# Kernel tuning notes

Hardware: AMD Instinct MI355X
Metric: run time of the kernel (lower is better)

The kernel has to match this reference:

```python
import jax, jax.numpy as jnp
import numpy as np

N = 50000      # nodes
E = 800000     # edges (before self loops)
D_IN = 128
D_H = 128
HEADS = 4
C = D_H // HEADS
D_OUT = 64
G = 50         # graphs in batch
EPS = 1e-5


def setup_inputs() -> dict:
    key = jax.random.key(0)
    ks = jax.random.split(key, 40)
    def rn(k, shape, scale=0.05):
        return jax.random.normal(k, shape, jnp.float32) * scale
    inp = {}
    inp['x'] = jax.random.normal(ks[0], (N, D_IN), jnp.float32)
    inp['edge_index'] = jax.random.randint(ks[1], (2, E), 0, N, dtype=jnp.int32)
    inp['batch'] = jnp.sort(jax.random.randint(ks[2], (N,), 0, G, dtype=jnp.int32))
    # GATConv 1 (in=D_IN, heads=4, out-per-head=C, concat)
    inp['gat1_W'] = rn(ks[3], (D_IN, D_H))
    inp['gat1_as'] = rn(ks[4], (HEADS, C))
    inp['gat1_ad'] = rn(ks[5], (HEADS, C))
    inp['gat1_b'] = rn(ks[6], (D_H,))
    # GATConv 2 (in=D_H)
    inp['gat2_W'] = rn(ks[7], (D_H, D_H))
    inp['gat2_as'] = rn(ks[8], (HEADS, C))
    inp['gat2_ad'] = rn(ks[9], (HEADS, C))
    inp['gat2_b'] = rn(ks[10], (D_H,))
    # SAGEConv 3/4/5: lin_l (aggregated neighbors, has bias), lin_r (root, no bias)
    for i, kk in zip((3, 4, 5), (11, 14, 17)):
        inp[f'sage{i}_Wl'] = rn(ks[kk], (D_H, D_H))
        inp[f'sage{i}_bl'] = rn(ks[kk + 1], (D_H,))
        inp[f'sage{i}_Wr'] = rn(ks[kk + 2], (D_H, D_H))
    # BatchNorms (training-mode batch statistics)
    for i in range(1, 6):
        inp[f'bn{i}_g'] = jnp.ones((D_H,), jnp.float32)
        inp[f'bn{i}_b'] = jnp.zeros((D_H,), jnp.float32)
    # residual projections + final fc
    inp['res1_W'] = rn(ks[20], (D_IN, D_H)); inp['res1_b'] = rn(ks[21], (D_H,))
    inp['res2_W'] = rn(ks[22], (D_H, D_H)); inp['res2_b'] = rn(ks[23], (D_H,))
    inp['fc_W'] = rn(ks[24], (D_H, D_OUT)); inp['fc_b'] = rn(ks[25], (D_OUT,))
    return inp


def _segsum(v, idx, n):
    return jax.ops.segment_sum(v, idx, num_segments=n)


def _gat(x, W, a_src, a_dst, b, src, dst):
    # PyG GATConv with self loops already appended to (src, dst).
    h = (x @ W).reshape(N, HEADS, C)
    es = jnp.einsum('nhc,hc->nh', h, a_src)           # [N,H]
    ed = jnp.einsum('nhc,hc->nh', h, a_dst)
    e = jax.nn.leaky_relu(es[src] + ed[dst], 0.2)     # [Etot,H]
    m = jax.ops.segment_max(e, dst, num_segments=N)
    m = jnp.where(jnp.isfinite(m), m, 0.0)
    w = jnp.exp(e - m[dst])
    z = _segsum(w, dst, N)
    alpha = w / jnp.maximum(z[dst], 1e-16)            # edge softmax over dst
    out = _segsum(h[src] * alpha[:, :, None], dst, N)  # [N,H,C]
    return out.reshape(N, D_H) + b


def _sage(x, Wl, bl, Wr, src, dst):
    # PyG SAGEConv(aggr='mean'): lin_l(mean_neighbors) + lin_r(x)
    deg = _segsum(jnp.ones((src.shape[0],), x.dtype), dst, N)
    mean = _segsum(x[src], dst, N) / jnp.maximum(deg, 1.0)[:, None]
    return mean @ Wl + bl + x @ Wr


def _bn(x, g, b):
    mu = x.mean(0)
    var = x.var(0)
    return g * (x - mu) * jax.lax.rsqrt(var + EPS) + b


def reference(x, edge_index, batch,
              gat1_W, gat1_as, gat1_ad, gat1_b,
              gat2_W, gat2_as, gat2_ad, gat2_b,
              sage3_Wl, sage3_bl, sage3_Wr,
              sage4_Wl, sage4_bl, sage4_Wr,
              sage5_Wl, sage5_bl, sage5_Wr,
              bn1_g, bn1_b, bn2_g, bn2_b, bn3_g, bn3_b, bn4_g, bn4_b, bn5_g, bn5_b,
              res1_W, res1_b, res2_W, res2_b, fc_W, fc_b):
    src, dst = edge_index[0], edge_index[1]
    loops = jnp.arange(N, dtype=edge_index.dtype)
    gsrc = jnp.concatenate([src, loops])   # GATConv adds self loops by default
    gdst = jnp.concatenate([dst, loops])
    lrelu = lambda v: jax.nn.leaky_relu(v, 0.2)

    res1 = x @ res1_W + res1_b
    h = _gat(x, gat1_W, gat1_as, gat1_ad, gat1_b, gsrc, gdst)
    h = lrelu(_bn(h, bn1_g, bn1_b) + res1)            # dropout = identity (eval)

    res2 = h @ res2_W + res2_b
    h = _gat(h, gat2_W, gat2_as, gat2_ad, gat2_b, gsrc, gdst)
    h = lrelu(_bn(h, bn2_g, bn2_b) + res2)

    h = lrelu(_bn(_sage(h, sage3_Wl, sage3_bl, sage3_Wr, src, dst), bn3_g, bn3_b))
    h = lrelu(_bn(_sage(h, sage4_Wl, sage4_bl, sage4_Wr, src, dst), bn4_g, bn4_b))
    h = lrelu(_bn(_sage(h, sage5_Wl, sage5_bl, sage5_Wr, src, dst), bn5_g, bn5_b))

    # global_mean_pool over graphs
    cnt = jax.ops.segment_sum(jnp.ones((N,), h.dtype), batch, num_segments=G)
    pooled = jax.ops.segment_sum(h, batch, num_segments=G) / jnp.maximum(cnt, 1.0)[:, None]
    return pooled @ fc_W + fc_b
```

## Files before the change

kernel.cpp:

```cpp
#include <hip/hip_runtime.h>
#include <math.h>
#include <stdint.h>

#define N_NODES 50000
#define N_EDGES 800000
#define D 128
#define GR 50
#define EPSV 1e-5f
#define GATGRID 2048

typedef __attribute__((ext_vector_type(8))) short bf16x8;
typedef __attribute__((ext_vector_type(4))) float f32x4;

__device__ __forceinline__ float lrelu(float v){ return v > 0.f ? v : 0.2f*v; }

__device__ __forceinline__ unsigned int f2bf(float f){
  union { float f; uint32_t i; } v; v.f = f;
  uint32_t r = v.i + 0x7fffu + ((v.i >> 16) & 1u);
  return r >> 16;
}
__device__ __forceinline__ float2 bf2f2(uint32_t u){
  union { uint32_t i; float f; } a, b;
  a.i = u << 16;
  b.i = u & 0xffff0000u;
  return make_float2(a.f, b.f);
}

__global__ void k_countrank(const int* __restrict__ dst, int* __restrict__ deg,
                            int* __restrict__ rank){
  int e = blockIdx.x*256 + threadIdx.x;
  if (e < N_EDGES) rank[e] = atomicAdd(&deg[dst[e]], 1);
}
__global__ void k_scan1(const int* __restrict__ deg, int* __restrict__ bsum){
  __shared__ int s[256];
  int i = blockIdx.x*256 + threadIdx.x;
  int v = (i < N_NODES) ? deg[i] : 0;
  s[threadIdx.x] = v; __syncthreads();
  for (int off = 128; off > 0; off >>= 1){
    if (threadIdx.x < off) s[threadIdx.x] += s[threadIdx.x + off];
    __syncthreads();
  }
  if (threadIdx.x == 0) bsum[blockIdx.x] = s[0];
}
__global__ void k_scan2b(int* __restrict__ bsum, int nb, int* __restrict__ rowStart){
  __shared__ int s[256];
  int t = threadIdx.x;
  int v = (t < nb) ? bsum[t] : 0;
  s[t] = v; __syncthreads();
  for (int off = 1; off < 256; off <<= 1){
    int xv = (t >= off) ? s[t - off] : 0;
    __syncthreads();
    s[t] += xv;
    __syncthreads();
  }
  if (t < nb) bsum[t] = s[t] - v;
  if (t == 255) rowStart[N_NODES] = s[255];
}
__global__ void k_scan3(const int* __restrict__ deg, const int* __restrict__ bsum,
                        int* __restrict__ rowStart){
  __shared__ int s[256];
  int i = blockIdx.x*256 + threadIdx.x;
  int v = (i < N_NODES) ? deg[i] : 0;
  s[threadIdx.x] = v; __syncthreads();
  for (int off = 1; off < 256; off <<= 1){
    int xv = (threadIdx.x >= off) ? s[threadIdx.x - off] : 0;
    __syncthreads();
    s[threadIdx.x] += xv;
    __syncthreads();
  }
  if (i < N_NODES) rowStart[i] = bsum[blockIdx.x] + s[threadIdx.x] - v;
}
__global__ void k_scatter(const int* __restrict__ src, const int* __restrict__ dst,
                          const int* __restrict__ rank, const int* __restrict__ rowStart,
                          int* __restrict__ srcList){
  int e = blockIdx.x*256 + threadIdx.x;
  if (e < N_EDGES)
    srcList[rowStart[dst[e]] + rank[e]] = src[e];
}

__global__ void k_cast_x(const float* __restrict__ x, unsigned short* __restrict__ x16){
  int idx = blockIdx.x*256 + threadIdx.x;
  if (idx >= N_NODES*32) return;
  float4 v = *(const float4*)(x + (size_t)idx*4);
  uint2 pk;
  pk.x = f2bf(v.x) | (f2bf(v.y) << 16);
  pk.y = f2bf(v.z) | (f2bf(v.w) << 16);
  *(uint2*)(x16 + (size_t)idx*4) = pk;
}

struct WPack { const float* w[10]; };
__global__ void k_castw(WPack p, unsigned short* __restrict__ wt){
  int mat = blockIdx.x >> 6;
  int local = (blockIdx.x & 63)*256 + threadIdx.x;
  int c = local >> 7, k = local & 127;
  wt[(size_t)mat*16384 + c*128 + k] = (unsigned short)f2bf(p.w[mat][k*128 + c]);
}

__device__ __forceinline__ void stage_w(const unsigned short* __restrict__ wt,
                                        unsigned short* __restrict__ lds, int t){
  #pragma unroll
  for (int i = 0; i < 8; ++i){
    int ch = i*256 + t;
    int col = ch >> 4, kc = ch & 15;
    *(uint4*)(&lds[col*136 + kc*8]) = *(const uint4*)(wt + ((size_t)col << 7) + (kc << 3));
  }
}

__device__ __forceinline__ void load_a(const unsigned short* __restrict__ xrow,
                                       int quad, bf16x8 a[4]){
  #pragma unroll
  for (int ks = 0; ks < 4; ++ks)
    a[ks] = *(const bf16x8*)(xrow + ks*32 + quad*8);
}

__device__ __forceinline__ void mfma_regs(const bf16x8 a[4],
                                          const unsigned short* __restrict__ lds,
                                          int lane, f32x4 acc[8]){
  int quad = lane >> 4, m = lane & 15;
  #pragma unroll
  for (int ks = 0; ks < 4; ++ks){
    #pragma unroll
    for (int nt = 0; nt < 8; ++nt){
      bf16x8 b = *(const bf16x8*)(&lds[(nt*16 + m)*136 + ks*32 + quad*8]);
      acc[nt] = __builtin_amdgcn_mfma_f32_16x16x32_bf16(a[ks], b, acc[nt], 0, 0, 0);
    }
  }
}

__device__ __forceinline__ void epi_store16(f32x4 acc[8], const float* bias,
    unsigned short* __restrict__ ldsw, unsigned short* __restrict__ Y16,
    int rbase, int lane, int n){
  int quad = lane >> 4, m = lane & 15;
  #pragma unroll
  for (int nt = 0; nt < 8; ++nt){
    int col = nt*16 + m;
    float bv = bias ? bias[col] : 0.f;
    #pragma unroll
    for (int reg = 0; reg < 4; ++reg)
      ldsw[(quad*4 + reg)*132 + col] = (unsigned short)f2bf(acc[nt][reg] + bv);
  }
  int r = lane >> 2, seg = lane & 3;
  int grow = rbase + r;
  if (grow < n){
    unsigned short* gp = Y16 + (size_t)grow*128 + seg*32;
    #pragma unroll
    for (int j = 0; j < 4; ++j)
      *(uint4*)(gp + j*8) = *(const uint4*)(&ldsw[r*132 + seg*32 + j*8]);
  }
}

__global__ __launch_bounds__(256) void k_mgemm_dual(const unsigned short* __restrict__ X16,
    const unsigned short* __restrict__ wtres, const unsigned short* __restrict__ wtgat,
    const float* __restrict__ bres, const float* __restrict__ as_,
    const float* __restrict__ ad_, unsigned short* __restrict__ R16,
    unsigned short* __restrict__ H16, float* __restrict__ es, float* __restrict__ ed,
    int n){
  __shared__ __align__(16) unsigned short Wlds[128*136];
  int t = threadIdx.x, lane = t & 63, w = t >> 6;
  int quad = lane >> 4, m = lane & 15;
  int rbase = blockIdx.x*64 + w*16;
  int rowA = rbase + m; if (rowA >= n) rowA = n - 1;
  bf16x8 a[4];
  load_a(X16 + (size_t)rowA*128, quad, a);
  stage_w(wtres, Wlds, t);
  f32x4 accR[8], accG[8];
  #pragma unroll
  for (int nt = 0; nt < 8; ++nt){
    accR[nt][0]=0.f; accR[nt][1]=0.f; accR[nt][2]=0.f; accR[nt][3]=0.f;
    accG[nt][0]=0.f; accG[nt][1]=0.f; accG[nt][2]=0.f; accG[nt][3]=0.f;
  }
  __syncthreads();
  mfma_regs(a, Wlds, lane, accR);
  __syncthreads();
  stage_w(wtgat, Wlds, t);
  __syncthreads();
  mfma_regs(a, Wlds, lane, accG);

  float asv[8], adv[8];
  #pragma unroll
  for (int nt = 0; nt < 8; ++nt){ asv[nt] = as_[nt*16 + m]; adv[nt] = ad_[nt*16 + m]; }
  #pragma unroll
  for (int reg = 0; reg < 4; ++reg){
    int row = rbase + quad*4 + reg;
    float pe[4], pd[4];
    #pragma unroll
    for (int h = 0; h < 4; ++h){
      pe[h] = accG[2*h][reg]*asv[2*h] + accG[2*h+1][reg]*asv[2*h+1];
      pd[h] = accG[2*h][reg]*adv[2*h] + accG[2*h+1][reg]*adv[2*h+1];
    }
    #pragma unroll
    for (int h = 0; h < 4; ++h){
      pe[h] += __shfl_xor(pe[h], 1); pe[h] += __shfl_xor(pe[h], 2);
      pe[h] += __shfl_xor(pe[h], 4); pe[h] += __shfl_xor(pe[h], 8);
      pd[h] += __shfl_xor(pd[h], 1); pd[h] += __shfl_xor(pd[h], 2);
      pd[h] += __shfl_xor(pd[h], 4); pd[h] += __shfl_xor(pd[h], 8);
    }
    if (m == 0 && row < n){
      #pragma unroll
      for (int h = 0; h < 4; ++h){ es[row*4 + h] = pe[h]; ed[row*4 + h] = pd[h]; }
    }
  }
  __syncthreads();
  epi_store16(accR, bres,    Wlds + w*2112, R16, rbase, lane, n);
  epi_store16(accG, nullptr, Wlds + w*2112, H16, rbase, lane, n);
}

__global__ __launch_bounds__(256) void k_mgemm2(const unsigned short* __restrict__ Xa,
    const unsigned short* __restrict__ wta, const unsigned short* __restrict__ Xb,
    const unsigned short* __restrict__ wtb, const float* __restrict__ bias,
    unsigned short* __restrict__ Y16, int n, float* __restrict__ bnpart){
  __shared__ __align__(16) unsigned short Wlds[128*136];
  __shared__ float wredS[4][128], wredQ[4][128];
  int t = threadIdx.x, lane = t & 63, w = t >> 6;
  int quad = lane >> 4, m = lane & 15;
  int rbase = blockIdx.x*64 + w*16;
  int rowA = rbase + m; if (rowA >= n) rowA = n - 1;
  bf16x8 aa[4], ab[4];
  load_a(Xa + (size_t)rowA*128, quad, aa);
  load_a(Xb + (size_t)rowA*128, quad, ab);
  stage_w(wta, Wlds, t);
  f32x4 acc[8];
  #pragma unroll
  for (int nt = 0; nt < 8; ++nt){ acc[nt][0]=0.f; acc[nt][1]=0.f; acc[nt][2]=0.f; acc[nt][3]=0.f; }
  __syncthreads();
  mfma_regs(aa, Wlds, lane, acc);
  __syncthreads();
  stage_w(wtb, Wlds, t);
  __syncthreads();
  mfma_regs(ab, Wlds, lane, acc);

  float colS[8], colQ[8];
  #pragma unroll
  for (int nt = 0; nt < 8; ++nt){
    float bv = bias[nt*16 + m];
    float s = 0.f, q = 0.f;
    #pragma unroll
    for (int reg = 0; reg < 4; ++reg){
      float o = acc[nt][reg] + bv;
      acc[nt][reg] = o;
      if (rbase + quad*4 + reg < n){ s += o; q += o*o; }
    }
    s += __shfl_xor(s, 16); s += __shfl_xor(s, 32);
    q += __shfl_xor(q, 16); q += __shfl_xor(q, 32);
    colS[nt] = s; colQ[nt] = q;
  }
  if (quad == 0){
    #pragma unroll
    for (int nt = 0; nt < 8; ++nt){
      wredS[w][nt*16 + m] = colS[nt];
      wredQ[w][nt*16 + m] = colQ[nt];
    }
  }
  __syncthreads();
  if (t < 128){
    float S = wredS[0][t] + wredS[1][t] + wredS[2][t] + wredS[3][t];
    float Q = wredQ[0][t] + wredQ[1][t] + wredQ[2][t] + wredQ[3][t];
    bnpart[(size_t)blockIdx.x*256 + t]       = S;
    bnpart[(size_t)blockIdx.x*256 + 128 + t] = Q;
  }
  epi_store16(acc, nullptr, Wlds + w*2112, Y16, rbase, lane, n);
}

__global__ void k_bnred(const float* __restrict__ part, int nblk,
                        float* __restrict__ sums){
  int g = blockIdx.x, t = threadIdx.x;
  int chunk = (nblk + 63) / 64;
  int b0 = g*chunk, b1 = min(nblk, b0 + chunk);
  float s = 0.f;
  for (int b = b0; b < b1; ++b) s += part[(size_t)b*256 + t];
  if (b0 < b1) atomicAdd(&sums[t], s);
}

__global__ __launch_bounds__(256) void k_gat(const uint4* __restrict__ h16,
    const float* __restrict__ es, const float* __restrict__ edv,
    const int* __restrict__ rowStart, const int* __restrict__ srcList,
    const float* __restrict__ bias, uint4* __restrict__ out16,
    float* __restrict__ bnpart){
  __shared__ float wredS[4][128], wredQ[4][128];
  int t = threadIdx.x;
  int lane = t & 63, wv = t >> 6;
  int sub = lane >> 4;
  int m   = lane & 15;
  int hd  = m >> 2;
  float4 bv0 = *(const float4*)(bias + m*8);
  float4 bv1 = *(const float4*)(bias + m*8 + 4);
  float colS[8], colQ[8];
  #pragma unroll
  for (int j = 0; j < 8; ++j){ colS[j] = 0.f; colQ[j] = 0.f; }

  for (int i = blockIdx.x*4 + wv; i < N_NODES; i += GATGRID*4){
    float edi = edv[i*4 + hd];
    float acc[8];
    #pragma unroll
    for (int j = 0; j < 8; ++j) acc[j] = 0.f;
    float z = 0.f;
    if (sub == 0){
      float ws = __expf(lrelu(es[i*4 + hd] + edi));
      uint4 u = h16[i*16 + m];
      float2 v0=bf2f2(u.x), v1=bf2f2(u.y), v2=bf2f2(u.z), v3=bf2f2(u.w);
      acc[0]=v0.x*ws; acc[1]=v0.y*ws; acc[2]=v1.x*ws; acc[3]=v1.y*ws;
      acc[4]=v2.x*ws; acc[5]=v2.y*ws; acc[6]=v3.x*ws; acc[7]=v3.y*ws;
      z = ws;
    }
    int k0 = rowStart[i], ke = rowStart[i + 1];
    for (int k = k0; k < ke; k += 8){
      int e0 = k + sub, e1 = k + 4 + sub;
      int c0 = e0 < ke ? e0 : ke - 1;
      int c1 = e1 < ke ? e1 : ke - 1;
      int s0 = srcList[c0];
      int s1 = srcList[c1];
      uint4 u0 = h16[s0*16 + m];
      uint4 u1 = h16[s1*16 + m];
      float w0 = (e0 < ke) ? __expf(lrelu(es[s0*4 + hd] + edi)) : 0.f;
      float w1 = (e1 < ke) ? __expf(lrelu(es[s1*4 + hd] + edi)) : 0.f;
      z += w0 + w1;
      float2 a0=bf2f2(u0.x), a1=bf2f2(u0.y), a2=bf2f2(u0.z), a3=bf2f2(u0.w);
      float2 b0=bf2f2(u1.x), b1=bf2f2(u1.y), b2=bf2f2(u1.z), b3=bf2f2(u1.w);
      acc[0] += a0.x*w0 + b0.x*w1;  acc[1] += a0.y*w0 + b0.y*w1;
      acc[2] += a1.x*w0 + b1.x*w1;  acc[3] += a1.y*w0 + b1.y*w1;
      acc[4] += a2.x*w0 + b2.x*w1;  acc[5] += a2.y*w0 + b2.y*w1;
      acc[6] += a3.x*w0 + b3.x*w1;  acc[7] += a3.y*w0 + b3.y*w1;
    }
    #pragma unroll
    for (int j = 0; j < 8; ++j){
      acc[j] += __shfl_xor(acc[j], 16);
      acc[j] += __shfl_xor(acc[j], 32);
    }
    z += __shfl_xor(z, 16);
    z += __shfl_xor(z, 32);
    if (sub == 0){
      float inv = 1.f / z;
      float o[8];
      o[0]=acc[0]*inv+bv0.x; o[1]=acc[1]*inv+bv0.y; o[2]=acc[2]*inv+bv0.z; o[3]=acc[3]*inv+bv0.w;
      o[4]=acc[4]*inv+bv1.x; o[5]=acc[5]*inv+bv1.y; o[6]=acc[6]*inv+bv1.z; o[7]=acc[7]*inv+bv1.w;
      #pragma unroll
      for (int j = 0; j < 8; ++j){ colS[j] += o[j]; colQ[j] += o[j]*o[j]; }
      uint4 pk;
      pk.x = f2bf(o[0]) | (f2bf(o[1]) << 16);
      pk.y = f2bf(o[2]) | (f2bf(o[3]) << 16);
      pk.z = f2bf(o[4]) | (f2bf(o[5]) << 16);
      pk.w = f2bf(o[6]) | (f2bf(o[7]) << 16);
      out16[i*16 + m] = pk;
    }
  }
  if (sub == 0){
    #pragma unroll
    for (int j = 0; j < 8; ++j){
      wredS[wv][m*8 + j] = colS[j];
      wredQ[wv][m*8 + j] = colQ[j];
    }
  }
  __syncthreads();
  if (t < 128){
    float S = wredS[0][t] + wredS[1][t] + wredS[2][t] + wredS[3][t];
    float Q = wredQ[0][t] + wredQ[1][t] + wredQ[2][t] + wredQ[3][t];
    bnpart[(size_t)blockIdx.x*256 + t]       = S;
    bnpart[(size_t)blockIdx.x*256 + 128 + t] = Q;
  }
}

__global__ __launch_bounds__(256) void k_sage_mean(const uint4* __restrict__ h16,
    const int* __restrict__ rowStart, const int* __restrict__ srcList,
    uint4* __restrict__ out16){
  int i = blockIdx.x*4 + (threadIdx.x >> 6);
  if (i >= N_NODES) return;
  int lane = threadIdx.x & 63;
  int sub = lane >> 4;
  int m   = lane & 15;
  float acc[8];
  #pragma unroll
  for (int j = 0; j < 8; ++j) acc[j] = 0.f;
  int k0 = rowStart[i], ke = rowStart[i + 1];
  for (int k = k0; k < ke; k += 8){
    int e0 = k + sub, e1 = k + 4 + sub;
    int c0 = e0 < ke ? e0 : ke - 1;
    int c1 = e1 < ke ? e1 : ke - 1;
    int s0 = srcList[c0];
    int s1 = srcList[c1];
    uint4 u0 = h16[s0*16 + m];
    uint4 u1 = h16[s1*16 + m];
    float w0 = (e0 < ke) ? 1.f : 0.f;
    float w1 = (e1 < ke) ? 1.f : 0.f;
    float2 a0=bf2f2(u0.x), a1=bf2f2(u0.y), a2=bf2f2(u0.z), a3=bf2f2(u0.w);
    float2 b0=bf2f2(u1.x), b1=bf2f2(u1.y), b2=bf2f2(u1.z), b3=bf2f2(u1.w);
    acc[0] += a0.x*w0 + b0.x*w1;  acc[1] += a0.y*w0 + b0.y*w1;
    acc[2] += a1.x*w0 + b1.x*w1;  acc[3] += a1.y*w0 + b1.y*w1;
    acc[4] += a2.x*w0 + b2.x*w1;  acc[5] += a2.y*w0 + b2.y*w1;
    acc[6] += a3.x*w0 + b3.x*w1;  acc[7] += a3.y*w0 + b3.y*w1;
  }
  #pragma unroll
  for (int j = 0; j < 8; ++j){
    acc[j] += __shfl_xor(acc[j], 16);
    acc[j] += __shfl_xor(acc[j], 32);
  }
  if (sub == 0){
    int dg = ke - k0;
    float inv = 1.f / (float)(dg > 0 ? dg : 1);
    uint4 pk;
    pk.x = f2bf(acc[0]*inv) | (f2bf(acc[1]*inv) << 16);
    pk.y = f2bf(acc[2]*inv) | (f2bf(acc[3]*inv) << 16);
    pk.z = f2bf(acc[4]*inv) | (f2bf(acc[5]*inv) << 16);
    pk.w = f2bf(acc[6]*inv) | (f2bf(acc[7]*inv) << 16);
    out16[i*16 + m] = pk;
  }
}

__global__ void k_bnapply(const unsigned int* __restrict__ x16,
    const float* __restrict__ sums, const float* __restrict__ g,
    const float* __restrict__ b, const unsigned int* __restrict__ res16,
    unsigned int* __restrict__ y16){
  int f = blockIdx.x*256 + threadIdx.x;
  if (f >= N_NODES*32) return;
  int c = (f & 31) * 4;
  uint2 u = *(const uint2*)(x16 + (size_t)f*2);
  float2 vA = bf2f2(u.x), vB = bf2f2(u.y);
  float vv[4] = {vA.x, vA.y, vB.x, vB.y};
  float rr[4] = {0.f, 0.f, 0.f, 0.f};
  if (res16){
    uint2 ur = *(const uint2*)(res16 + (size_t)f*2);
    float2 rA = bf2f2(ur.x), rB = bf2f2(ur.y);
    rr[0]=rA.x; rr[1]=rA.y; rr[2]=rB.x; rr[3]=rB.y;
  }
  float o[4];
  const float invn = 1.f / (float)N_NODES;
  #pragma unroll
  for (int j = 0; j < 4; ++j){
    int cc = c + j;
    float mu  = sums[cc] * invn;
    float var = sums[128 + cc] * invn - mu*mu;
    float rs  = rsqrtf(var + EPSV);
    o[j] = lrelu((vv[j] - mu)*rs*g[cc] + b[cc] + rr[j]);
  }
  uint2 pk;
  pk.x = f2bf(o[0]) | (f2bf(o[1]) << 16);
  pk.y = f2bf(o[2]) | (f2bf(o[3]) << 16);
  *(uint2*)(y16 + (size_t)f*2) = pk;
}

__global__ __launch_bounds__(256) void k_pool(const unsigned int* __restrict__ h16,
    const int* __restrict__ batch, float* __restrict__ pooled,
    float* __restrict__ cnt){
  int colu = threadIdx.x & 63;
  int ro   = threadIdx.x >> 6;
  int base = blockIdx.x * 128;
  int g_cur = -1; float a0 = 0.f, a1 = 0.f, cacc = 0.f;
  for (int ii = 0; ii < 32; ++ii){
    int r = base + ro + ii*4;
    if (r >= N_NODES) break;
    int g = batch[r];
    if (g != g_cur){
      if (g_cur >= 0){
        atomicAdd(&pooled[g_cur*D + 2*colu],     a0);
        atomicAdd(&pooled[g_cur*D + 2*colu + 1], a1);
        if (colu == 0) atomicAdd(&cnt[g_cur], cacc);
      }
      a0 = 0.f; a1 = 0.f; cacc = 0.f; g_cur = g;
    }
    float2 v = bf2f2(h16[(size_t)r*64 + colu]);
    a0 += v.x; a1 += v.y; cacc += 1.f;
  }
  if (g_cur >= 0){
    atomicAdd(&pooled[g_cur*D + 2*colu],     a0);
    atomicAdd(&pooled[g_cur*D + 2*colu + 1], a1);
    if (colu == 0) atomicAdd(&cnt[g_cur], cacc);
  }
}

__global__ void k_fc(const float* __restrict__ pooled, const float* __restrict__ cnt,
    const float* __restrict__ W, const float* __restrict__ b, float* __restrict__ out){
  int idx = blockIdx.x*256 + threadIdx.x;
  if (idx >= GR*64) return;
  int g = idx >> 6, o = idx & 63;
  const float* p = pooled + g*D;
  float s = 0.f;
  for (int c2 = 0; c2 < D; ++c2) s += p[c2] * W[c2*64 + o];
  float inv = 1.f / fmaxf(cnt[g], 1.f);
  out[idx] = s*inv + b[o];
}

extern "C" void kernel_launch(void* const* d_in, const int* in_sizes, int n_in,
                              void* d_out, int out_size, void* d_ws, size_t ws_size,
                              hipStream_t stream){
  (void)in_sizes; (void)n_in; (void)out_size; (void)ws_size;
  const float* x       = (const float*)d_in[0];
  const int*   ei      = (const int*)  d_in[1];
  const int*   batch   = (const int*)  d_in[2];
  const float* gat1_W  = (const float*)d_in[3];
  const float* gat1_as = (const float*)d_in[4];
  const float* gat1_ad = (const float*)d_in[5];
  const float* gat1_b  = (const float*)d_in[6];
  const float* gat2_W  = (const float*)d_in[7];
  const float* gat2_as = (const float*)d_in[8];
  const float* gat2_ad = (const float*)d_in[9];
  const float* gat2_b  = (const float*)d_in[10];
  const float* s3_Wl   = (const float*)d_in[11];
  const float* s3_bl   = (const float*)d_in[12];
  const float* s3_Wr   = (const float*)d_in[13];
  const float* s4_Wl   = (const float*)d_in[14];
  const float* s4_bl   = (const float*)d_in[15];
  const float* s4_Wr   = (const float*)d_in[16];
  const float* s5_Wl   = (const float*)d_in[17];
  const float* s5_bl   = (const float*)d_in[18];
  const float* s5_Wr   = (const float*)d_in[19];
  const float* bn1_g = (const float*)d_in[20]; const float* bn1_b = (const float*)d_in[21];
  const float* bn2_g = (const float*)d_in[22]; const float* bn2_b = (const float*)d_in[23];
  const float* bn3_g = (const float*)d_in[24]; const float* bn3_b = (const float*)d_in[25];
  const float* bn4_g = (const float*)d_in[26]; const float* bn4_b = (const float*)d_in[27];
  const float* bn5_g = (const float*)d_in[28]; const float* bn5_b = (const float*)d_in[29];
  const float* res1_W = (const float*)d_in[30]; const float* res1_b = (const float*)d_in[31];
  const float* res2_W = (const float*)d_in[32]; const float* res2_b = (const float*)d_in[33];
  const float* fc_W   = (const float*)d_in[34]; const float* fc_b   = (const float*)d_in[35];
  float* out = (float*)d_out;

  char* ws = (char*)d_ws;
  size_t off = 0;
  auto alloc = [&](size_t bytes) -> void* {
    void* p = ws + off; off += (bytes + 255) & ~(size_t)255; return p;
  };
  const int mgrid = (N_NODES + 63) / 64;
  int*   rowStart = (int*)  alloc((N_NODES + 1) * 4);
  int*   deg      = (int*)  alloc((size_t)N_NODES * 4);
  int*   rank     = (int*)  alloc((size_t)N_EDGES * 4);
  int*   srcList  = (int*)  alloc((size_t)N_EDGES * 4);
  int*   bsum     = (int*)  alloc(256 * 4);
  float* bnsums   = (float*)alloc(5 * 256 * 4);
  float* pooled   = (float*)alloc(GR * D * 4);
  float* cnt      = (float*)alloc(64 * 4);
  float* es       = (float*)alloc((size_t)N_NODES * 4 * 4);
  float* edv      = (float*)alloc((size_t)N_NODES * 4 * 4);
  float* bnpart   = (float*)alloc((size_t)GATGRID * 256 * 4);
  unsigned short* Wt16 = (unsigned short*)alloc(10 * 16384 * 2);
  unsigned short* HX   = (unsigned short*)alloc((size_t)N_NODES * D * 2);
  unsigned short* H16a = (unsigned short*)alloc((size_t)N_NODES * D * 2);
  unsigned short* HO   = (unsigned short*)alloc((size_t)N_NODES * D * 2);
  unsigned short* HR   = (unsigned short*)alloc((size_t)N_NODES * D * 2);

  const int* srcE = ei;
  const int* dstE = ei + N_EDGES;
  const int nb = (N_NODES + 255) / 256;
  const int egrid = (N_EDGES + 255) / 256;
  const int agrid = (N_NODES + 3) / 4;
  const int bgrid = (N_NODES*32 + 255) / 256;
  const int pgrid = (N_NODES + 127) / 128;

  hipMemsetAsync(deg, 0, (size_t)N_NODES*4, stream);
  hipMemsetAsync(bnsums, 0, (5*256 + GR*D + 64)*4, stream);
  k_countrank<<<egrid, 256, 0, stream>>>(dstE, deg, rank);
  k_scan1<<<nb, 256, 0, stream>>>(deg, bsum);
  k_scan2b<<<1, 256, 0, stream>>>(bsum, nb, rowStart);
  k_scan3<<<nb, 256, 0, stream>>>(deg, bsum, rowStart);
  k_scatter<<<egrid, 256, 0, stream>>>(srcE, dstE, rank, rowStart, srcList);

  WPack wp;
  wp.w[0]=res1_W; wp.w[1]=gat1_W; wp.w[2]=res2_W; wp.w[3]=gat2_W;
  wp.w[4]=s3_Wl;  wp.w[5]=s3_Wr;  wp.w[6]=s4_Wl;  wp.w[7]=s4_Wr;
  wp.w[8]=s5_Wl;  wp.w[9]=s5_Wr;
  k_castw<<<640, 256, 0, stream>>>(wp, Wt16);
  k_cast_x<<<bgrid, 256, 0, stream>>>(x, HX);

  k_mgemm_dual<<<mgrid, 256, 0, stream>>>(HX, Wt16 + 0*16384, Wt16 + 1*16384,
                                          res1_b, gat1_as, gat1_ad,
                                          HR, H16a, es, edv, N_NODES);
  k_gat<<<GATGRID, 256, 0, stream>>>((const uint4*)H16a, es, edv, rowStart,
                                     srcList, gat1_b, (uint4*)HO, bnpart);
  k_bnred<<<64, 256, 0, stream>>>(bnpart, GATGRID, bnsums);
  k_bnapply<<<bgrid, 256, 0, stream>>>((const unsigned int*)HO, bnsums, bn1_g, bn1_b,
                                       (const unsigned int*)HR, (unsigned int*)H16a);

  k_mgemm_dual<<<mgrid, 256, 0, stream>>>(H16a, Wt16 + 2*16384, Wt16 + 3*16384,
                                          res2_b, gat2_as, gat2_ad,
                                          HR, HX, es, edv, N_NODES);
  k_gat<<<GATGRID, 256, 0, stream>>>((const uint4*)HX, es, edv, rowStart,
                                     srcList, gat2_b, (uint4*)HO, bnpart);
  k_bnred<<<64, 256, 0, stream>>>(bnpart, GATGRID, bnsums + 256);
  k_bnapply<<<bgrid, 256, 0, stream>>>((const unsigned int*)HO, bnsums + 256, bn2_g, bn2_b,
                                       (const unsigned int*)HR, (unsigned int*)H16a);

  k_sage_mean<<<agrid, 256, 0, stream>>>((const uint4*)H16a, rowStart, srcList,
                                         (uint4*)HX);
  k_mgemm2<<<mgrid, 256, 0, stream>>>(HX, Wt16 + 4*16384, H16a, Wt16 + 5*16384,
                                      s3_bl, HO, N_NODES, bnpart);
  k_bnred<<<64, 256, 0, stream>>>(bnpart, mgrid, bnsums + 512);
  k_bnapply<<<bgrid, 256, 0, stream>>>((const unsigned int*)HO, bnsums + 512, bn3_g, bn3_b,
                                       nullptr, (unsigned int*)H16a);

  k_sage_mean<<<agrid, 256, 0, stream>>>((const uint4*)H16a, rowStart, srcList,
                                         (uint4*)HX);
  k_mgemm2<<<mgrid, 256, 0, stream>>>(HX, Wt16 + 6*16384, H16a, Wt16 + 7*16384,
                                      s4_bl, HO, N_NODES, bnpart);
  k_bnred<<<64, 256, 0, stream>>>(bnpart, mgrid, bnsums + 768);
  k_bnapply<<<bgrid, 256, 0, stream>>>((const unsigned int*)HO, bnsums + 768, bn4_g, bn4_b,
                                       nullptr, (unsigned int*)H16a);

  k_sage_mean<<<agrid, 256, 0, stream>>>((const uint4*)H16a, rowStart, srcList,
                                         (uint4*)HX);
  k_mgemm2<<<mgrid, 256, 0, stream>>>(HX, Wt16 + 8*16384, H16a, Wt16 + 9*16384,
                                      s5_bl, HO, N_NODES, bnpart);
  k_bnred<<<64, 256, 0, stream>>>(bnpart, mgrid, bnsums + 1024);
  k_bnapply<<<bgrid, 256, 0, stream>>>((const unsigned int*)HO, bnsums + 1024, bn5_g, bn5_b,
                                       nullptr, (unsigned int*)H16a);

  k_pool<<<pgrid, 256, 0, stream>>>((const unsigned int*)H16a, batch, pooled, cnt);
  k_fc<<<(GR*64 + 255)/256, 256, 0, stream>>>(pooled, cnt, fc_W, fc_b, out);
}
```

Baseline: 611.2 us.

## Unfuse BN statistics from GAT kernel and launch one wave per node

The GAT aggregation kernel drops its persistent grid-stride loop and fused batch-norm column sums, so each wave handles exactly one node and blocks exit early. A new k_bnstat kernel re-reads the bf16 output and accumulates per-column sum and sum-of-squares with atomics, replacing the bnpart/k_bnred path for the GAT layers. This aims to improve load balance and occupancy in the irregular gather kernel at the cost of an extra 12.8 MB read pass. Statistics are now computed from bf16-rounded outputs rather than fp32 values, which slightly changes numerics.

```diff
diff --git a/kernel.cpp b/kernel.cpp
--- a/kernel.cpp
+++ b/kernel.cpp
@@ -7,7 +7,6 @@
 #define D 128
 #define GR 50
 #define EPSV 1e-5f
-#define GATGRID 2048
 
 typedef __attribute__((ext_vector_type(8))) short bf16x8;
 typedef __attribute__((ext_vector_type(4))) float f32x4;
@@ -274,88 +273,62 @@
 __global__ __launch_bounds__(256) void k_gat(const uint4* __restrict__ h16,
     const float* __restrict__ es, const float* __restrict__ edv,
     const int* __restrict__ rowStart, const int* __restrict__ srcList,
-    const float* __restrict__ bias, uint4* __restrict__ out16,
-    float* __restrict__ bnpart){
-  __shared__ float wredS[4][128], wredQ[4][128];
-  int t = threadIdx.x;
-  int lane = t & 63, wv = t >> 6;
+    const float* __restrict__ bias, uint4* __restrict__ out16){
+  int i = blockIdx.x*4 + (threadIdx.x >> 6);
+  if (i >= N_NODES) return;
+  int lane = threadIdx.x & 63;
   int sub = lane >> 4;
   int m   = lane & 15;
   int hd  = m >> 2;
-  float4 bv0 = *(const float4*)(bias + m*8);
-  float4 bv1 = *(const float4*)(bias + m*8 + 4);
-  float colS[8], colQ[8];
-  #pragma unroll
-  for (int j = 0; j < 8; ++j){ colS[j] = 0.f; colQ[j] = 0.f; }
-
-  for (int i = blockIdx.x*4 + wv; i < N_NODES; i += GATGRID*4){
-    float edi = edv[i*4 + hd];
-    float acc[8];
-    #pragma unroll
-    for (int j = 0; j < 8; ++j) acc[j] = 0.f;
-    float z = 0.f;
-    if (sub == 0){
-      float ws = __expf(lrelu(es[i*4 + hd] + edi));
-      uint4 u = h16[i*16 + m];
-      float2 v0=bf2f2(u.x), v1=bf2f2(u.y), v2=bf2f2(u.z), v3=bf2f2(u.w);
-      acc[0]=v0.x*ws; acc[1]=v0.y*ws; acc[2]=v1.x*ws; acc[3]=v1.y*ws;
-      acc[4]=v2.x*ws; acc[5]=v2.y*ws; acc[6]=v3.x*ws; acc[7]=v3.y*ws;
-      z = ws;
-    }
-    int k0 = rowStart[i], ke = rowStart[i + 1];
-    for (int k = k0; k < ke; k += 8){
-      int e0 = k + sub, e1 = k + 4 + sub;
-      int c0 = e0 < ke ? e0 : ke - 1;
-      int c1 = e1 < ke ? e1 : ke - 1;
-      int s0 = srcList[c0];
-      int s1 = srcList[c1];
-      uint4 u0 = h16[s0*16 + m];
-      uint4 u1 = h16[s1*16 + m];
-      float w0 = (e0 < ke) ? __expf(lrelu(es[s0*4 + hd] + edi)) : 0.f;
-      float w1 = (e1 < ke) ? __expf(lrelu(es[s1*4 + hd] + edi)) : 0.f;
-      z += w0 + w1;
-      float2 a0=bf2f2(u0.x), a1=bf2f2(u0.y), a2=bf2f2(u0.z), a3=bf2f2(u0.w);
-      float2 b0=bf2f2(u1.x), b1=bf2f2(u1.y), b2=bf2f2(u1.z), b3=bf2f2(u1.w);
-      acc[0] += a0.x*w0 + b0.x*w1;  acc[1] += a0.y*w0 + b0.y*w1;
-      acc[2] += a1.x*w0 + b1.x*w1;  acc[3] += a1.y*w0 + b1.y*w1;
-      acc[4] += a2.x*w0 + b2.x*w1;  acc[5] += a2.y*w0 + b2.y*w1;
-      acc[6] += a3.x*w0 + b3.x*w1;  acc[7] += a3.y*w0 + b3.y*w1;
-    }
-    #pragma unroll
-    for (int j = 0; j < 8; ++j){
-      acc[j] += __shfl_xor(acc[j], 16);
-      acc[j] += __shfl_xor(acc[j], 32);
-    }
-    z += __shfl_xor(z, 16);
-    z += __shfl_xor(z, 32);
-    if (sub == 0){
-      float inv = 1.f / z;
-      float o[8];
-      o[0]=acc[0]*inv+bv0.x; o[1]=acc[1]*inv+bv0.y; o[2]=acc[2]*inv+bv0.z; o[3]=acc[3]*inv+bv0.w;
-      o[4]=acc[4]*inv+bv1.x; o[5]=acc[5]*inv+bv1.y; o[6]=acc[6]*inv+bv1.z; o[7]=acc[7]*inv+bv1.w;
-      #pragma unroll
-      for (int j = 0; j < 8; ++j){ colS[j] += o[j]; colQ[j] += o[j]*o[j]; }
-      uint4 pk;
-      pk.x = f2bf(o[0]) | (f2bf(o[1]) << 16);
-      pk.y = f2bf(o[2]) | (f2bf(o[3]) << 16);
-      pk.z = f2bf(o[4]) | (f2bf(o[5]) << 16);
-      pk.w = f2bf(o[6]) | (f2bf(o[7]) << 16);
-      out16[i*16 + m] = pk;
-    }
-  }
+  float edi = edv[i*4 + hd];
+  float acc[8];
+  #pragma unroll
+  for (int j = 0; j < 8; ++j) acc[j] = 0.f;
+  float z = 0.f;
   if (sub == 0){
-    #pragma unroll
-    for (int j = 0; j < 8; ++j){
-      wredS[wv][m*8 + j] = colS[j];
-      wredQ[wv][m*8 + j] = colQ[j];
-    }
-  }
-  __syncthreads();
-  if (t < 128){
-    float S = wredS[0][t] + wredS[1][t] + wredS[2][t] + wredS[3][t];
-    float Q = wredQ[0][t] + wredQ[1][t] + wredQ[2][t] + wredQ[3][t];
-    bnpart[(size_t)blockIdx.x*256 + t]       = S;
-    bnpart[(size_t)blockIdx.x*256 + 128 + t] = Q;
+    float ws = __expf(lrelu(es[i*4 + hd] + edi));
+    uint4 u = h16[i*16 + m];
+    float2 v0=bf2f2(u.x), v1=bf2f2(u.y), v2=bf2f2(u.z), v3=bf2f2(u.w);
+    acc[0]=v0.x*ws; acc[1]=v0.y*ws; acc[2]=v1.x*ws; acc[3]=v1.y*ws;
+    acc[4]=v2.x*ws; acc[5]=v2.y*ws; acc[6]=v3.x*ws; acc[7]=v3.y*ws;
+    z = ws;
+  }
+  int k0 = rowStart[i], ke = rowStart[i + 1];
+  for (int k = k0; k < ke; k += 8){
+    int e0 = k + sub, e1 = k + 4 + sub;
+    int c0 = e0 < ke ? e0 : ke - 1;
+    int c1 = e1 < ke ? e1 : ke - 1;
+    int s0 = srcList[c0];
+    int s1 = srcList[c1];
+    uint4 u0 = h16[s0*16 + m];
+    uint4 u1 = h16[s1*16 + m];
+    float w0 = (e0 < ke) ? __expf(lrelu(es[s0*4 + hd] + edi)) : 0.f;
+    float w1 = (e1 < ke) ? __expf(lrelu(es[s1*4 + hd] + edi)) : 0.f;
+    z += w0 + w1;
+    float2 a0=bf2f2(u0.x), a1=bf2f2(u0.y), a2=bf2f2(u0.z), a3=bf2f2(u0.w);
+    float2 b0=bf2f2(u1.x), b1=bf2f2(u1.y), b2=bf2f2(u1.z), b3=bf2f2(u1.w);
+    acc[0] += a0.x*w0 + b0.x*w1;  acc[1] += a0.y*w0 + b0.y*w1;
+    acc[2] += a1.x*w0 + b1.x*w1;  acc[3] += a1.y*w0 + b1.y*w1;
+    acc[4] += a2.x*w0 + b2.x*w1;  acc[5] += a2.y*w0 + b2.y*w1;
+    acc[6] += a3.x*w0 + b3.x*w1;  acc[7] += a3.y*w0 + b3.y*w1;
+  }
+  #pragma unroll
+  for (int j = 0; j < 8; ++j){
+    acc[j] += __shfl_xor(acc[j], 16);
+    acc[j] += __shfl_xor(acc[j], 32);
+  }
+  z += __shfl_xor(z, 16);
+  z += __shfl_xor(z, 32);
+  if (sub == 0){
+    float inv = 1.f / z;
+    float4 bv0 = *(const float4*)(bias + m*8);
+    float4 bv1 = *(const float4*)(bias + m*8 + 4);
+    uint4 pk;
+    pk.x = f2bf(acc[0]*inv + bv0.x) | (f2bf(acc[1]*inv + bv0.y) << 16);
+    pk.y = f2bf(acc[2]*inv + bv0.z) | (f2bf(acc[3]*inv + bv0.w) << 16);
+    pk.z = f2bf(acc[4]*inv + bv1.x) | (f2bf(acc[5]*inv + bv1.y) << 16);
+    pk.w = f2bf(acc[6]*inv + bv1.z) | (f2bf(acc[7]*inv + bv1.w) << 16);
+    out16[i*16 + m] = pk;
   }
 }
 
@@ -402,6 +375,31 @@
     pk.z = f2bf(acc[4]*inv) | (f2bf(acc[5]*inv) << 16);
     pk.w = f2bf(acc[6]*inv) | (f2bf(acc[7]*inv) << 16);
     out16[i*16 + m] = pk;
+  }
+}
+
+__global__ __launch_bounds__(256) void k_bnstat(const unsigned int* __restrict__ x16,
+                                                float* __restrict__ sums){
+  int colu = threadIdx.x & 63;
+  int ro   = threadIdx.x >> 6;
+  float s0 = 0.f, s1 = 0.f, q0 = 0.f, q1 = 0.f;
+  for (int r = blockIdx.x*4 + ro; r < N_NODES; r += gridDim.x*4){
+    float2 v = bf2f2(x16[(size_t)r*64 + colu]);
+    s0 += v.x; s1 += v.y; q0 += v.x*v.x; q1 += v.y*v.y;
+  }
+  __shared__ float rs0[256], rs1[256], rq0[256], rq1[256];
+  int t = threadIdx.x;
+  rs0[t] = s0; rs1[t] = s1; rq0[t] = q0; rq1[t] = q1;
+  __syncthreads();
+  if (t < 64){
+    float S0 = rs0[t] + rs0[t+64] + rs0[t+128] + rs0[t+192];
+    float S1 = rs1[t] + rs1[t+64] + rs1[t+128] + rs1[t+192];
+    float Q0 = rq0[t] + rq0[t+64] + rq0[t+128] + rq0[t+192];
+    float Q1 = rq1[t] + rq1[t+64] + rq1[t+128] + rq1[t+192];
+    atomicAdd(&sums[2*t],       S0);
+    atomicAdd(&sums[2*t + 1],   S1);
+    atomicAdd(&sums[128 + 2*t],     Q0);
+    atomicAdd(&sums[128 + 2*t + 1], Q1);
   }
 }
 
@@ -528,7 +526,7 @@
   float* cnt      = (float*)alloc(64 * 4);
   float* es       = (float*)alloc((size_t)N_NODES * 4 * 4);
   float* edv      = (float*)alloc((size_t)N_NODES * 4 * 4);
-  float* bnpart   = (float*)alloc((size_t)GATGRID * 256 * 4);
+  float* bnpart   = (float*)alloc((size_t)mgrid * 256 * 4);
   unsigned short* Wt16 = (unsigned short*)alloc(10 * 16384 * 2);
   unsigned short* HX   = (unsigned short*)alloc((size_t)N_NODES * D * 2);
   unsigned short* H16a = (unsigned short*)alloc((size_t)N_NODES * D * 2);
@@ -561,18 +559,18 @@
   k_mgemm_dual<<<mgrid, 256, 0, stream>>>(HX, Wt16 + 0*16384, Wt16 + 1*16384,
                                           res1_b, gat1_as, gat1_ad,
                                           HR, H16a, es, edv, N_NODES);
-  k_gat<<<GATGRID, 256, 0, stream>>>((const uint4*)H16a, es, edv, rowStart,
-                                     srcList, gat1_b, (uint4*)HO, bnpart);
-  k_bnred<<<64, 256, 0, stream>>>(bnpart, GATGRID, bnsums);
+  k_gat<<<agrid, 256, 0, stream>>>((const uint4*)H16a, es, edv, rowStart,
+                                   srcList, gat1_b, (uint4*)HO);
+  k_bnstat<<<256, 256, 0, stream>>>((const unsigned int*)HO, bnsums);
   k_bnapply<<<bgrid, 256, 0, stream>>>((const unsigned int*)HO, bnsums, bn1_g, bn1_b,
                                        (const unsigned int*)HR, (unsigned int*)H16a);
 
   k_mgemm_dual<<<mgrid, 256, 0, stream>>>(H16a, Wt16 + 2*16384, Wt16 + 3*16384,
                                           res2_b, gat2_as, gat2_ad,
                                           HR, HX, es, edv, N_NODES);
-  k_gat<<<GATGRID, 256, 0, stream>>>((const uint4*)HX, es, edv, rowStart,
-                                     srcList, gat2_b, (uint4*)HO, bnpart);
-  k_bnred<<<64, 256, 0, stream>>>(bnpart, GATGRID, bnsums + 256);
+  k_gat<<<agrid, 256, 0, stream>>>((const uint4*)HX, es, edv, rowStart,
+                                   srcList, gat2_b, (uint4*)HO);
+  k_bnstat<<<256, 256, 0, stream>>>((const unsigned int*)HO, bnsums + 256);
   k_bnapply<<<bgrid, 256, 0, stream>>>((const unsigned int*)HO, bnsums + 256, bn2_g, bn2_b,
                                        (const unsigned int*)HR, (unsigned int*)H16a);
 
```

After: 614.7 us. About the same (+0.6%).
